# Performance work log

Hardware: AMD Instinct MI355X
Metric: run time of the kernel (lower is better)

## Reference

```python
import jax, jax.numpy as jnp
from jax import lax
import numpy as np

NEG_SLOPE = 0.01  # nn.LeakyReLU default
D_K = 2.0

def conv_block(x, W, b, pad, pool_k, pool_s):
    # Conv2d -> MaxPool2d -> Dropout(p=0, identity) -> LeakyReLU
    y = lax.conv_general_dilated(x, W, window_strides=(1, 1),
                                 padding=[(pad, pad), (pad, pad)],
                                 dimension_numbers=('NCHW', 'OIHW', 'NCHW'))
    y = y + b[None, :, None, None]
    y = lax.reduce_window(y, -jnp.inf, lax.max,
                          (1, 1, pool_k, pool_k), (1, 1, pool_s, pool_s), 'VALID')
    return jnp.where(y > 0, y, NEG_SLOPE * y)

def setup_inputs() -> dict:
    key = jax.random.key(0)
    ks = jax.random.split(key, 12)
    d = {}
    d['X'] = jax.random.normal(ks[0], (8, 30, 3, 200, 200), jnp.float32)
    d['W1'] = jax.random.normal(ks[1], (16, 3, 9, 9), jnp.float32) * 0.05
    d['b1'] = jnp.zeros((16,), jnp.float32)
    d['W2'] = jax.random.normal(ks[2], (32, 16, 7, 7), jnp.float32) * 0.03
    d['b2'] = jnp.zeros((32,), jnp.float32)
    d['W3'] = jax.random.normal(ks[3], (64, 32, 5, 5), jnp.float32) * 0.03
    d['b3'] = jnp.zeros((64,), jnp.float32)
    # 16 heads stacked; torch init is torch.rand (uniform [0,1))
    d['Wq'] = jax.random.uniform(ks[4], (16, 256, 2), jnp.float32)
    d['Wk'] = jax.random.uniform(ks[5], (16, 256, 2), jnp.float32)
    d['Wv'] = jax.random.uniform(ks[6], (16, 256, 4), jnp.float32)
    d['Wr'] = jax.random.normal(ks[7], (10, 1920), jnp.float32) * 0.02
    d['br'] = jnp.zeros((10,), jnp.float32)
    return d

def reference(X, W1, b1, W2, b2, W3, b3, Wq, Wk, Wv, Wr, br):
    B, T = X.shape[0], X.shape[1]
    Y = X.reshape(B * T, X.shape[2], X.shape[3], X.shape[4])
    Y = conv_block(Y, W1, b1, pad=1, pool_k=7, pool_s=5)   # [BT,16,38,38]
    Y = conv_block(Y, W2, b2, pad=0, pool_k=5, pool_s=3)   # [BT,32,10,10]
    Y = conv_block(Y, W3, b3, pad=0, pool_k=3, pool_s=2)   # [BT,64,2,2]
    Y = Y.reshape(B, T, -1)                                # [B,30,256]
    # batched multi-head self-attention (h=16, d_q=d_k=2, d_v=4)
    Q = jnp.einsum('bse,heq->bhsq', Y, Wq)
    K = jnp.einsum('bse,hek->bhsk', Y, Wk)
    V = jnp.einsum('bse,hev->bhsv', Y, Wv)
    omega = jnp.einsum('bhsq,bhtq->bhst', Q, K) / (D_K ** 0.5)
    # original: F.softmax(omega, dim=0) on a [S,S] per-sample matrix -> query axis
    alpha = jax.nn.softmax(omega, axis=-2)
    Z = jnp.einsum('bhst,bhtv->bhsv', alpha, V)            # [B,16,30,4]
    Z = jnp.transpose(Z, (0, 2, 1, 3)).reshape(B, T, -1)   # concat heads, [B,30,64]
    out = Z.reshape(B, -1) @ Wr.T + br                     # [B,10]
    return jax.nn.softmax(out, axis=1)
```

## Files before the change

kernel.cpp:

```cpp
#include <hip/hip_runtime.h>
#include <hip/hip_bf16.h>
#include <math.h>

#define LEAKY(x) ((x) > 0.0f ? (x) : 0.01f*(x))

typedef __attribute__((ext_vector_type(8))) short bfrag8;
typedef __attribute__((ext_vector_type(16))) float accv16;

__device__ __forceinline__ unsigned short bfr(float x) {
  unsigned int u = __float_as_uint(x);
  unsigned int r = u + 0x7fffu + ((u >> 16) & 1u);
  return (unsigned short)(r >> 16);
}

__device__ __forceinline__ unsigned int b2u(__hip_bfloat162 v) {
  union { __hip_bfloat162 b; unsigned int u; } x; x.b = v; return x.u;
}

#define KMAP(lh, j) (8*((j)>>2) + 4*(lh) + ((j)&3))

__global__ __launch_bounds__(256) void prep_weights(
    const float* __restrict__ W2, const float* __restrict__ W3,
    const float* __restrict__ W1,
    float* __restrict__ w3r, unsigned short* __restrict__ bfrag,
    unsigned short* __restrict__ bfrag2)
{
  int i = blockIdx.x*256 + threadIdx.x;
  if (i < 51200) {
    int co = i & 63; int k = i >> 6;
    w3r[k*64 + co] = W3[co*800 + k];
  }
  if (i < 1280) {
    int lane = i & 63;
    int f = i >> 6;
    int hl = f / 10;
    int rem = f - hl*10;
    int kwh = rem >> 1;
    int ks  = rem & 1;
    int nn = lane & 31;
    int co = nn & 15, p = nn >> 4;
    int lh = (lane >> 5) & 1;
    #pragma unroll
    for (int j = 0; j < 8; ++j) {
      int k = ks*16 + KMAP(lh, j);
      float wv = 0.f;
      if (k < 27) {
        int ci = k / 9, kh = k - ci*9;
        int kw = 2*kwh + p;
        if (kw <= 8) wv = W1[((co*3 + ci)*9 + kh)*9 + kw];
      }
      unsigned short h = bfr(wv);
      unsigned short outv;
      if (hl == 0) outv = h;
      else {
        float hf = __uint_as_float(((unsigned int)h) << 16);
        outv = bfr(wv - hf);
      }
      bfrag[(f*64 + lane)*8 + j] = outv;
    }
  }
  if (i < 50176) {
    int j = i & 7;
    int f = i >> 3;
    int lane = f & 63;
    int g = f >> 6;
    int hl = g & 1;
    int t2 = g >> 1;
    int ks = t2 % 7, kw = t2 / 7;
    int co = lane & 31;
    int lh = (lane >> 5) & 1;
    int k = ks*16 + KMAP(lh, j);
    int ci = k / 7, kh = k - ci*7;
    float wv = W2[((co*16 + ci)*7 + kh)*7 + kw];
    unsigned short h = bfr(wv);
    if (hl == 0) bfrag2[i] = h;
    else {
      float hf = __uint_as_float(((unsigned int)h) << 16);
      bfrag2[i] = bfr(wv - hf);
    }
  }
}

__global__ __launch_bounds__(512, 2) void conv1_mfma(
    const float* __restrict__ X, const float* __restrict__ b1,
    const unsigned short* __restrict__ bfrag, float* __restrict__ out1)
{
  const int pr = blockIdx.x;
  const int n  = blockIdx.y;
  const int tid = threadIdx.x;
  const int lane = tid & 63;
  const int w = tid >> 6;

  __shared__ __align__(16) unsigned short plh[2][2][208][8];
  __shared__ __align__(16) unsigned short pll[2][2][208][8];
  __shared__ float rowbuf[193][2][16];
  __shared__ float pm[38][17];

  bfrag8 Bf[20];
  #pragma unroll
  for (int f = 0; f < 20; ++f)
    Bf[f] = *(const bfrag8*)&bfrag[(f*64 + lane)*8];

  for (int t = tid; t < 608; t += 512)
    pm[t >> 4][t & 15] = -INFINITY;

  const float* __restrict__ Xn = X + (size_t)n * 120000;

  for (int ph = 0; ph < 7; ++ph) {
    const int r = 5*pr + ph;

    for (int t = tid; t < 832; t += 512) {
      int q = t / 208;
      int c = t - q*208;
      int ks = q >> 1, lh = q & 1;
      int colX = c - 1;
      bool cok = (unsigned)colX < 200u;
      float xv[8];
      #pragma unroll
      for (int j = 0; j < 8; ++j) {
        int k = ks*16 + KMAP(lh, j);
        float x = 0.f;
        if (k < 27) {
          int ci = (k * 57) >> 9;
          int kh = k - ci*9;
          int row = r - 1 + kh;
          if (cok && (unsigned)row < 200u)
            x = Xn[(ci*200 + row)*200 + colX];
        }
        xv[j] = x;
      }
      unsigned int hh[4], ll[4];
      #pragma unroll
      for (int pq = 0; pq < 4; ++pq) {
        float x0 = xv[2*pq], x1 = xv[2*pq + 1];
        unsigned int h01 = b2u(__float22bfloat162_rn(make_float2(x0, x1)));
        float f0 = __uint_as_float(h01 << 16);
        float f1 = __uint_as_float(h01 & 0xffff0000u);
        unsigned int l01 = b2u(__float22bfloat162_rn(make_float2(x0 - f0, x1 - f1)));
        hh[pq] = h01; ll[pq] = l01;
      }
      *(uint4*)&plh[ks][lh][c][0] = make_uint4(hh[0], hh[1], hh[2], hh[3]);
      *(uint4*)&pll[ks][lh][c][0] = make_uint4(ll[0], ll[1], ll[2], ll[3]);
    }
    __syncthreads();

    if (w < 7) {
      const int m0 = w*32;
      const int lh = (lane >> 5) & 1;
      const int mi = lane & 31;
      accv16 C;
      #pragma unroll
      for (int e = 0; e < 16; ++e) C[e] = 0.f;

      #pragma unroll
      for (int ks = 0; ks < 2; ++ks) {
        #pragma unroll
        for (int kwh = 0; kwh < 5; ++kwh) {
          int col = m0 + mi + 2*kwh;
          col = col > 207 ? 207 : col;
          bfrag8 ah = *(const bfrag8*)&plh[ks][lh][col][0];
          bfrag8 al = *(const bfrag8*)&pll[ks][lh][col][0];
          C = __builtin_amdgcn_mfma_f32_32x32x16_bf16(ah, Bf[kwh*2 + ks],      C, 0, 0, 0);
          C = __builtin_amdgcn_mfma_f32_32x32x16_bf16(ah, Bf[10 + kwh*2 + ks], C, 0, 0, 0);
          C = __builtin_amdgcn_mfma_f32_32x32x16_bf16(al, Bf[kwh*2 + ks],      C, 0, 0, 0);
        }
      }
      const int co = lane & 15, p = (lane >> 4) & 1;
      #pragma unroll
      for (int reg = 0; reg < 16; ++reg) {
        int m = m0 + (reg & 3) + 8*(reg >> 2) + 4*lh;
        if (m < 193) rowbuf[m][p][co] = C[reg];
      }
    }
    __syncthreads();

    for (int t = tid; t < 304; t += 512) {
      int c2 = t & 7, pc = t >> 3;
      int u0 = 5*pc;
      float s0 = -INFINITY, s1 = -INFINITY;
      #pragma unroll
      for (int pw = 0; pw < 7; ++pw) {
        const float* r0 = &rowbuf[u0+pw][0][c2*2];
        const float* r1 = &rowbuf[u0+pw+1][1][c2*2];
        float v0 = r0[0] + r1[0];
        float v1 = r0[1] + r1[1];
        s0 = fmaxf(s0, v0); s1 = fmaxf(s1, v1);
      }
      pm[pc][c2*2]   = fmaxf(pm[pc][c2*2],   s0);
      pm[pc][c2*2+1] = fmaxf(pm[pc][c2*2+1], s1);
    }
    __syncthreads();
  }

  for (int t = tid; t < 608; t += 512) {
    int co = t & 15, pc = t >> 4;
    float v = pm[pc][co] + b1[co];
    out1[((n*16 + co)*38 + pr)*38 + pc] = LEAKY(v);
  }
}

__global__ __launch_bounds__(512, 1) void conv2_mfma(
    const float* __restrict__ in, const float* __restrict__ b2,
    const unsigned short* __restrict__ bfrag2, float* __restrict__ out2)
{
  const int py = blockIdx.x;
  const int n  = blockIdx.y;
  const int tid = threadIdx.x;
  const int lane = tid & 63;
  const int w = tid >> 6;

  __shared__ __align__(16) unsigned short p2h[7][2][200][8];
  __shared__ __align__(16) unsigned short p2l[7][2][200][8];
  __shared__ float rowbuf[224][32];

  for (int t = tid; t < 2800; t += 512) {
    int col = t % 200;
    int q   = t / 200;
    int ks  = q >> 1, lhh = q & 1;
    int ph  = col / 40;
    int c   = col - ph*40;
    bool cok = c < 38;
    int rbase = 3*py + ph;
    float xv[8];
    #pragma unroll
    for (int j = 0; j < 8; ++j) {
      int k = ks*16 + KMAP(lhh, j);
      int ci = k / 7;
      int kh = k - ci*7;
      xv[j] = cok ? in[((n*16 + ci)*38 + (rbase + kh))*38 + c] : 0.f;
    }
    unsigned int hh[4], ll[4];
    #pragma unroll
    for (int pq = 0; pq < 4; ++pq) {
      float x0 = xv[2*pq], x1 = xv[2*pq + 1];
      unsigned int h01 = b2u(__float22bfloat162_rn(make_float2(x0, x1)));
      float f0 = __uint_as_float(h01 << 16);
      float f1 = __uint_as_float(h01 & 0xffff0000u);
      unsigned int l01 = b2u(__float22bfloat162_rn(make_float2(x0 - f0, x1 - f1)));
      hh[pq] = h01; ll[pq] = l01;
    }
    *(uint4*)&p2h[ks][lhh][col][0] = make_uint4(hh[0], hh[1], hh[2], hh[3]);
    *(uint4*)&p2l[ks][lhh][col][0] = make_uint4(ll[0], ll[1], ll[2], ll[3]);
  }
  __syncthreads();

  if (w < 7) {
    const int m0 = w*32;
    const int lh = (lane >> 5) & 1;
    const int mi = lane & 31;
    accv16 C;
    #pragma unroll
    for (int e = 0; e < 16; ++e) C[e] = 0.f;

    for (int ks = 0; ks < 7; ++ks) {
      bfrag8 Bh[7], Bl[7];
      #pragma unroll
      for (int kw = 0; kw < 7; ++kw) {
        int t2 = kw*7 + ks;
        Bh[kw] = *(const bfrag8*)&bfrag2[((t2*2 + 0)*64 + lane)*8];
        Bl[kw] = *(const bfrag8*)&bfrag2[((t2*2 + 1)*64 + lane)*8];
      }
      #pragma unroll
      for (int kw = 0; kw < 7; ++kw) {
        int col = m0 + mi + kw;
        col = col > 199 ? 199 : col;
        bfrag8 ah = *(const bfrag8*)&p2h[ks][lh][col][0];
        bfrag8 al = *(const bfrag8*)&p2l[ks][lh][col][0];
        C = __builtin_amdgcn_mfma_f32_32x32x16_bf16(ah, Bh[kw], C, 0, 0, 0);
        C = __builtin_amdgcn_mfma_f32_32x32x16_bf16(ah, Bl[kw], C, 0, 0, 0);
        C = __builtin_amdgcn_mfma_f32_32x32x16_bf16(al, Bh[kw], C, 0, 0, 0);
      }
    }
    const int co = lane & 31;
    #pragma unroll
    for (int reg = 0; reg < 16; ++reg) {
      int m = m0 + (reg & 3) + 8*(reg >> 2) + 4*((lane >> 5) & 1);
      rowbuf[m][co] = C[reg];
    }
  }
  __syncthreads();

  for (int t = tid; t < 320; t += 512) {
    int co = t & 31, pc = t >> 5;
    float m = -INFINITY;
    #pragma unroll
    for (int ph = 0; ph < 5; ++ph)
      #pragma unroll
      for (int pw = 0; pw < 5; ++pw)
        m = fmaxf(m, rowbuf[ph*40 + 3*pc + pw][co]);
    float v = m + b2[co];
    out2[((n*32 + co)*10 + py)*10 + pc] = LEAKY(v);
  }
}

__global__ __launch_bounds__(256) void conv3_pool(
    const float* __restrict__ in, const float* __restrict__ w3r,
    const float* __restrict__ b3, float* __restrict__ out3)
{
  const int n = blockIdx.x;
  __shared__ float sIn[3200];
  const int tid = threadIdx.x;
  for (int idx = tid; idx < 3200; idx += 256)
    sIn[idx] = in[n*3200 + idx];
  __syncthreads();
  const int co  = tid & 63;
  const int pos = tid >> 6;
  const int py = pos >> 1, px = pos & 1;
  float acc[3][3];
  float bv = b3[co];
  #pragma unroll
  for (int dy = 0; dy < 3; ++dy)
    #pragma unroll
    for (int dx = 0; dx < 3; ++dx) acc[dy][dx] = bv;
  for (int ci = 0; ci < 32; ++ci) {
    for (int kh = 0; kh < 5; ++kh) {
      float xr[3][7];
      #pragma unroll
      for (int dy = 0; dy < 3; ++dy)
        #pragma unroll
        for (int cc = 0; cc < 7; ++cc)
          xr[dy][cc] = sIn[ci*100 + (2*py + kh + dy)*10 + (2*px + cc)];
      #pragma unroll
      for (int kw = 0; kw < 5; ++kw) {
        float wv = w3r[(ci*25 + kh*5 + kw)*64 + co];
        #pragma unroll
        for (int dy = 0; dy < 3; ++dy)
          #pragma unroll
          for (int dx = 0; dx < 3; ++dx)
            acc[dy][dx] = fmaf(xr[dy][dx + kw], wv, acc[dy][dx]);
      }
    }
  }
  float m = -INFINITY;
  #pragma unroll
  for (int dy = 0; dy < 3; ++dy)
    #pragma unroll
    for (int dx = 0; dx < 3; ++dx) m = fmaxf(m, acc[dy][dx]);
  out3[n*256 + co*4 + py*2 + px] = LEAKY(m);
}

__global__ __launch_bounds__(64) void attn_kernel(
    const float* __restrict__ Y, const float* __restrict__ Wq,
    const float* __restrict__ Wk, const float* __restrict__ Wv,
    float* __restrict__ Zc)
{
  const int h = blockIdx.x;
  const int b = blockIdx.y;
  __shared__ float sQ[30][2], sK[30][2], sV[30][4], sA[30][30];
  const int t = threadIdx.x;
  for (int it = t; it < 240; it += 64) {
    if (it < 60) {
      int s = it >> 1, q = it & 1;
      const float* yp = &Y[(b*30 + s)*256];
      const float* wp = &Wq[h*512 + q];
      float acc = 0.f;
      for (int e = 0; e < 256; ++e) acc += yp[e]*wp[e*2];
      sQ[s][q] = acc;
    } else if (it < 120) {
      int rr = it - 60;
      int s = rr >> 1, q = rr & 1;
      const float* yp = &Y[(b*30 + s)*256];
      const float* wp = &Wk[h*512 + q];
      float acc = 0.f;
      for (int e = 0; e < 256; ++e) acc += yp[e]*wp[e*2];
      sK[s][q] = acc;
    } else {
      int rr = it - 120;
      int s = rr >> 2, v = rr & 3;
      const float* yp = &Y[(b*30 + s)*256];
      const float* wp = &Wv[h*1024 + v];
      float acc = 0.f;
      for (int e = 0; e < 256; ++e) acc += yp[e]*wp[e*4];
      sV[s][v] = acc;
    }
  }
  __syncthreads();
  for (int it = t; it < 900; it += 64) {
    int si = it / 30, tj = it - si*30;
    sA[si][tj] = (sQ[si][0]*sK[tj][0] + sQ[si][1]*sK[tj][1]) * 0.70710678118654752f;
  }
  __syncthreads();
  if (t < 30) {
    float m = -INFINITY;
    for (int si = 0; si < 30; ++si) m = fmaxf(m, sA[si][t]);
    float sum = 0.f;
    for (int si = 0; si < 30; ++si) {
      float v = expf(sA[si][t] - m);
      sA[si][t] = v;
      sum += v;
    }
    float inv = 1.f/sum;
    for (int si = 0; si < 30; ++si) sA[si][t] *= inv;
  }
  __syncthreads();
  for (int it = t; it < 120; it += 64) {
    int si = it >> 2, v = it & 3;
    float z = 0.f;
    for (int tt = 0; tt < 30; ++tt) z += sA[si][tt]*sV[tt][v];
    Zc[(b*30 + si)*64 + h*4 + v] = z;
  }
}

__global__ __launch_bounds__(256) void head_kernel(
    const float* __restrict__ Zc, const float* __restrict__ Wr,
    const float* __restrict__ br, float* __restrict__ out)
{
  const int b = blockIdx.x;
  __shared__ float red[240];
  __shared__ float logit[10];
  const int t = threadIdx.x;
  if (t < 240) {
    int o = t / 24, j = t - o*24;
    const float* zp = &Zc[b*1920 + j*80];
    const float* wp = &Wr[o*1920 + j*80];
    float s = 0.f;
    for (int k = 0; k < 80; ++k) s += zp[k]*wp[k];
    red[t] = s;
  }
  __syncthreads();
  if (t < 10) {
    float s = br[t];
    #pragma unroll
    for (int j = 0; j < 24; ++j) s += red[t*24 + j];
    logit[t] = s;
  }
  __syncthreads();
  if (t == 0) {
    float m = -INFINITY;
    for (int o = 0; o < 10; ++o) m = fmaxf(m, logit[o]);
    float sum = 0.f;
    float ex[10];
    for (int o = 0; o < 10; ++o) { ex[o] = expf(logit[o] - m); sum += ex[o]; }
    float inv = 1.f/sum;
    for (int o = 0; o < 10; ++o) out[b*10 + o] = ex[o]*inv;
  }
}

extern "C" void kernel_launch(void* const* d_in, const int* in_sizes, int n_in,
                              void* d_out, int out_size, void* d_ws, size_t ws_size,
                              hipStream_t stream) {
  const float* X  = (const float*)d_in[0];
  const float* W1 = (const float*)d_in[1];
  const float* b1 = (const float*)d_in[2];
  const float* W2 = (const float*)d_in[3];
  const float* b2 = (const float*)d_in[4];
  const float* W3 = (const float*)d_in[5];
  const float* b3 = (const float*)d_in[6];
  const float* Wq = (const float*)d_in[7];
  const float* Wk = (const float*)d_in[8];
  const float* Wv = (const float*)d_in[9];
  const float* Wr = (const float*)d_in[10];
  const float* br = (const float*)d_in[11];

  float* ws  = (float*)d_ws;
  float* w3r = ws;
  unsigned short* bfrag  = (unsigned short*)(ws + 51200);
  unsigned short* bfrag2 = (unsigned short*)(ws + 56320);
  float* o1  = ws + 81408;
  float* o2  = ws + 5626368;
  float* o3  = ws + 6394368;
  float* zc  = ws + 6455808;

  prep_weights<<<dim3(200), dim3(256), 0, stream>>>(W2, W3, W1, w3r, bfrag, bfrag2);
  conv1_mfma  <<<dim3(38, 240), dim3(512), 0, stream>>>(X, b1, bfrag, o1);
  conv2_mfma  <<<dim3(10, 240), dim3(512), 0, stream>>>(o1, b2, bfrag2, o2);
  conv3_pool  <<<dim3(240),     dim3(256), 0, stream>>>(o2, w3r, b3, o3);
  attn_kernel <<<dim3(16, 8),   dim3(64),  0, stream>>>(o3, Wq, Wk, Wv, zc);
  head_kernel <<<dim3(8),       dim3(256), 0, stream>>>(zc, Wr, br, (float*)d_out);
}
```

Before: 761.1 us.

## Vectorize conv1 input staging with float4 loads and XOR-swizzled LDS layout

```diff
diff --git a/kernel.cpp b/kernel.cpp
--- a/kernel.cpp
+++ b/kernel.cpp
@@ -91,8 +91,8 @@
   const int lane = tid & 63;
   const int w = tid >> 6;
 
-  __shared__ __align__(16) unsigned short plh[2][2][208][8];
-  __shared__ __align__(16) unsigned short pll[2][2][208][8];
+  __shared__ __align__(128) unsigned short plh[4*208*8];
+  __shared__ __align__(128) unsigned short pll[4*208*8];
   __shared__ float rowbuf[193][2][16];
   __shared__ float pm[38][17];
 
@@ -101,46 +101,52 @@
   for (int f = 0; f < 20; ++f)
     Bf[f] = *(const bfrag8*)&bfrag[(f*64 + lane)*8];
 
+  {
+    uint4 z = make_uint4(0,0,0,0);
+    for (int t = tid; t < 832; t += 512) {
+      ((uint4*)plh)[t] = z;
+      ((uint4*)pll)[t] = z;
+    }
+  }
   for (int t = tid; t < 608; t += 512)
     pm[t >> 4][t & 15] = -INFINITY;
+  __syncthreads();
 
   const float* __restrict__ Xn = X + (size_t)n * 120000;
 
   for (int ph = 0; ph < 7; ++ph) {
-    const int r = 5*pr + ph;
-
-    for (int t = tid; t < 832; t += 512) {
-      int q = t / 208;
-      int c = t - q*208;
-      int ks = q >> 1, lh = q & 1;
-      int colX = c - 1;
-      bool cok = (unsigned)colX < 200u;
-      float xv[8];
-      #pragma unroll
-      for (int j = 0; j < 8; ++j) {
-        int k = ks*16 + KMAP(lh, j);
-        float x = 0.f;
+    if (w < 7 && lane < 50) {
+      const int q  = w >> 1;
+      const int jh = w & 1;
+      const int ks = q >> 1, lh2 = q & 1;
+      float xv[4][4];
+      #pragma unroll
+      for (int jj = 0; jj < 4; ++jj) {
+        int k = ks*16 + 8*jh + 4*lh2 + jj;
+        float4 v = make_float4(0.f, 0.f, 0.f, 0.f);
         if (k < 27) {
-          int ci = (k * 57) >> 9;
-          int kh = k - ci*9;
-          int row = r - 1 + kh;
-          if (cok && (unsigned)row < 200u)
-            x = Xn[(ci*200 + row)*200 + colX];
+          int ci = k / 9, kh = k - ci*9;
+          int row = 5*pr + ph - 1 + kh;
+          if (row >= 0)
+            v = *(const float4*)&Xn[(ci*200 + row)*200 + lane*4];
         }
-        xv[j] = x;
-      }
-      unsigned int hh[4], ll[4];
-      #pragma unroll
-      for (int pq = 0; pq < 4; ++pq) {
-        float x0 = xv[2*pq], x1 = xv[2*pq + 1];
-        unsigned int h01 = b2u(__float22bfloat162_rn(make_float2(x0, x1)));
+        xv[jj][0] = v.x; xv[jj][1] = v.y; xv[jj][2] = v.z; xv[jj][3] = v.w;
+      }
+      #pragma unroll
+      for (int t = 0; t < 4; ++t) {
+        int c = 4*lane + 1 + t;
+        unsigned int sidx = ((unsigned)((q*208 + c)*8 + jh*4)) ^ (unsigned)(c & 56);
+        unsigned int h01 = b2u(__float22bfloat162_rn(make_float2(xv[0][t], xv[1][t])));
+        unsigned int h23 = b2u(__float22bfloat162_rn(make_float2(xv[2][t], xv[3][t])));
         float f0 = __uint_as_float(h01 << 16);
         float f1 = __uint_as_float(h01 & 0xffff0000u);
-        unsigned int l01 = b2u(__float22bfloat162_rn(make_float2(x0 - f0, x1 - f1)));
-        hh[pq] = h01; ll[pq] = l01;
-      }
-      *(uint4*)&plh[ks][lh][c][0] = make_uint4(hh[0], hh[1], hh[2], hh[3]);
-      *(uint4*)&pll[ks][lh][c][0] = make_uint4(ll[0], ll[1], ll[2], ll[3]);
+        float f2 = __uint_as_float(h23 << 16);
+        float f3 = __uint_as_float(h23 & 0xffff0000u);
+        unsigned int l01 = b2u(__float22bfloat162_rn(make_float2(xv[0][t] - f0, xv[1][t] - f1)));
+        unsigned int l23 = b2u(__float22bfloat162_rn(make_float2(xv[2][t] - f2, xv[3][t] - f3)));
+        *(uint2*)&plh[sidx] = make_uint2(h01, h23);
+        *(uint2*)&pll[sidx] = make_uint2(l01, l23);
+      }
     }
     __syncthreads();
 
@@ -158,8 +164,10 @@
         for (int kwh = 0; kwh < 5; ++kwh) {
           int col = m0 + mi + 2*kwh;
           col = col > 207 ? 207 : col;
-          bfrag8 ah = *(const bfrag8*)&plh[ks][lh][col][0];
-          bfrag8 al = *(const bfrag8*)&pll[ks][lh][col][0];
+          unsigned int q2 = (unsigned)(ks*2 + lh);
+          unsigned int bidx = ((q2*208 + (unsigned)col)*8) ^ (unsigned)(col & 56);
+          bfrag8 ah = *(const bfrag8*)&plh[bidx];
+          bfrag8 al = *(const bfrag8*)&pll[bidx];
           C = __builtin_amdgcn_mfma_f32_32x32x16_bf16(ah, Bf[kwh*2 + ks],      C, 0, 0, 0);
           C = __builtin_amdgcn_mfma_f32_32x32x16_bf16(ah, Bf[10 + kwh*2 + ks], C, 0, 0, 0);
           C = __builtin_amdgcn_mfma_f32_32x32x16_bf16(al, Bf[kwh*2 + ks],      C, 0, 0, 0);
```

After: 1.004 ms. 31.9% more time.
